# Optimization experiments

Hardware: AMD Instinct MI355X
Metric: run time of the kernel (lower is better)

## Reference

```python
import jax, jax.numpy as jnp
import numpy as np
import math

EPS = 1e-11

def _gaussian_kernel3():
    # fixed 3x3 gaussian, mean=(3-1)/2=1, variance=0.5^2
    coords = jnp.arange(3, dtype=jnp.float32)
    xg = jnp.tile(coords[None, :], (3, 1))  # x_cord.repeat(3).view(3,3)
    yg = xg.T
    variance = 0.25
    g = (1.0 / (2.0 * math.pi * variance)) * jnp.exp(-((xg - 1.0) ** 2 + (yg - 1.0) ** 2) / (2.0 * variance))
    return g  # (3,3)

def setup_inputs() -> dict:
    key = jax.random.key(0)
    k1, k2 = jax.random.split(key)
    b, cin, h, w = 8, 512, 16, 16
    cout = 128
    x = jax.random.normal(k1, (b, cin, h, w), dtype=jnp.float32)
    w_conv = jax.random.normal(k2, (cout, cin), dtype=jnp.float32) * (1.0 / np.sqrt(cin))
    return {"x": x, "w_conv": w_conv}

def reference(x, w_conv):
    # 1x1 conv (no bias) + relu
    y = jnp.einsum('bihw,oi->bohw', x, w_conv)
    y = jax.nn.relu(y)
    # depthwise 3x3 gaussian blur, VALID padding (matches nn.Conv2d default padding=0)
    c = w_conv.shape[0]
    gk = _gaussian_kernel3()
    dw = jnp.tile(gk[None, None], (c, 1, 1, 1))  # (C,1,3,3)
    y = jax.lax.conv_general_dilated(
        y, dw, window_strides=(1, 1), padding='VALID',
        dimension_numbers=('NCHW', 'OIHW', 'NCHW'), feature_group_count=c)
    b, c, h, w = y.shape
    hw = h * w
    xf = y.reshape(b, c, hw)
    # shifted copies: xs[b, ch, i, p] = xf[b, ch, (p - i) mod hw]
    p = jnp.arange(hw)
    idx = (p[None, :] - p[:, None]) % hw  # (hw_i, hw_p)
    xs = xf[:, :, idx]  # [b, c, hw, hw]
    # responses[b, ch1, ch2, p] = sum_i xf[b,ch1,i] * xf[b,ch2,(p-i)%hw]
    R = jnp.einsum('bai,bcip->bacp', xf, xs)  # [b, c, c, hw]
    # faithful torch reshape: [b, c, c*hw] -> view(b, hw, c*c), max over dim 1
    resp = R.reshape(b, hw, c * c)
    c_ij = jnp.sqrt(jnp.max(resp, axis=1))  # [b, c*c]
    norm = jnp.sum(c_ij ** 2, axis=1, keepdims=True) + EPS
    return c_ij / norm
```

## Files before the change

### kernel.cpp

```cpp
#include <hip/hip_runtime.h>
#include <hip/hip_bf16.h>

typedef __bf16 bf16x8 __attribute__((ext_vector_type(8)));
typedef float floatx4 __attribute__((ext_vector_type(4)));
typedef unsigned short u16;
typedef unsigned int u32;

#define HW 196
#define NB 8
#define NC 128
#define CL 480
#define WROW 12544

#define OFF_XFRSW 0
#define OFF_XFE   458752
#define OFF_W     8323072
#define OFF_SUMS  21168128
#define OFF_YPART 21168160

__global__ __launch_bounds__(512) void k_conv(const float* __restrict__ x,
                                              const float* __restrict__ wc,
                                              float* __restrict__ Ypart) {
  const int b  = blockIdx.x;
  const int og = blockIdx.y;
  const int ks = blockIdx.z;
  const int t  = threadIdx.x;
  const int pix  = t & 255;
  const int half = t >> 8;

  const float* xb = x + ((size_t)(b * 512 + ks * 64 + half * 32)) * 256 + pix;
  const float* wp = wc + (og * 16) * 512 + ks * 64 + half * 32;

  float acc[16];
#pragma unroll
  for (int r = 0; r < 16; ++r) acc[r] = 0.f;
#pragma unroll 8
  for (int i = 0; i < 32; ++i) {
    float xv = xb[(size_t)i * 256];
#pragma unroll
    for (int r = 0; r < 16; ++r) acc[r] = fmaf(xv, wp[r * 512 + i], acc[r]);
  }

  __shared__ float red[16][512];
#pragma unroll
  for (int r = 0; r < 16; ++r) red[r][t] = acc[r];
  __syncthreads();

  if (t < 256) {
    float* yo = Ypart + (((size_t)(b * 8 + og) * 8 + ks) * 16) * 256 + t;
#pragma unroll
    for (int r = 0; r < 16; ++r)
      yo[r * 256] = red[r][t] + red[r][t + 256];
  }
}

__global__ __launch_bounds__(256) void k_reduce(const float* __restrict__ Ypart,
                                                uint4* __restrict__ xfr_sw,
                                                u16* __restrict__ xfe) {
  const int b  = blockIdx.x;
  const int rg = blockIdx.y;
  const int t  = threadIdx.x;

  __shared__ float ybuf[4][256];
  __shared__ u16 ydup[4][592];

#pragma unroll
  for (int oo = 0; oo < 4; ++oo) {
    const int o  = rg * 4 + oo;
    const int og = o >> 4, r = o & 15;
    const float* yp = Ypart + (((size_t)(b * 8 + og) * 8) * 16 + r) * 256 + t;
    float s = 0.f;
#pragma unroll
    for (int ks = 0; ks < 8; ++ks) s += yp[(size_t)ks * 16 * 256];
    ybuf[oo][t] = fmaxf(s, 0.f);
  }
  __syncthreads();

  const float GC = 0.63661977236758138f;
  const float GE = GC * 0.13533528323661270f;
  const float GD = GC * 0.018315638888734179f;

  if (t < HW) {
    const int h = t / 14, w2 = t - h * 14;
#pragma unroll
    for (int oo = 0; oo < 4; ++oo) {
      const float* yb = &ybuf[oo][h * 16 + w2];
      float v = GD * (yb[0] + yb[2] + yb[32] + yb[34])
              + GE * (yb[1] + yb[16] + yb[18] + yb[33])
              + GC * yb[17];
      union { __hip_bfloat16 h2; u16 u; } cv; cv.h2 = __float2bfloat16(v);
      ydup[oo][t] = cv.u; ydup[oo][t + 196] = cv.u; ydup[oo][t + 392] = cv.u;
    }
  }
  __syncthreads();

  if (t < 112) {
    const int oo = t / 28;
    const int g  = t - oo * 28;
    const int kb = g >> 2, quad = g & 3;
    const int c  = rg * 4 + oo;
    const int at = c >> 4, m = c & 15;
    union { u16 u[8]; uint4 v; } pk;
#pragma unroll
    for (int j = 0; j < 8; ++j) {
      const int k = g * 8 + j;
      pk.u[j] = (k < HW) ? ydup[oo][HW - k] : (u16)0;
    }
    xfr_sw[b * 3584 + ((kb * 8 + at) * 4 + quad) * 16 + m] = pk.v;
  }

  uint4* xfe4 = (uint4*)xfe;
  for (int idx = t; idx < 4 * 8 * 60; idx += 256) {
    const int oo = idx / 480;
    const int rem = idx - oo * 480;
    const int S = rem / 60;
    const int g = rem - S * 60;
    const int c = rg * 4 + oo;
    union { u16 u[8]; uint4 v; } pk;
#pragma unroll
    for (int j = 0; j < 8; ++j) pk.u[j] = ydup[oo][g * 8 + j + S];
    xfe4[((size_t)(b * NC + c) * 8 + S) * 60 + g] = pk.v;
  }
}

__global__ __launch_bounds__(256, 2) void k_cooc(const uint4* __restrict__ xfr_sw,
                                                 const u16* __restrict__ xfe,
                                                 u32* __restrict__ W) {
  const int b     = blockIdx.x;
  const int cpair = blockIdx.y;
  const int t     = threadIdx.x;

  __shared__ __align__(16) uint4 Abuf[3584];
  __shared__ __align__(16) u16 Obuf[32 * 200];

  {
    const uint4* src = xfr_sw + b * 3584;
    for (int j = t; j < 3584; j += 256) Abuf[j] = src[j];
  }
  __syncthreads();

  const int lane = t & 63;
  const int wv   = t >> 6;
  const int n    = lane & 15;
  const int quad = lane >> 4;
  const u16* xbase = xfe + ((size_t)(b * NC) * 8) * CL + (n & 8) + quad * 8
                   + (size_t)(n & 7) * CL;

  for (int c2 = 0; c2 < 2; ++c2) {
    const int c = cpair * 2 + c2;
    const u16* xc = xbase + (size_t)c * (8 * CL);

    floatx4 acc[8][4];
#pragma unroll
    for (int at = 0; at < 8; ++at)
#pragma unroll
      for (int j = 0; j < 4; ++j) acc[at][j] = (floatx4){0.f, 0.f, 0.f, 0.f};

    for (int kb = 0; kb < 7; ++kb) {
      bf16x8 af[8];
#pragma unroll
      for (int at = 0; at < 8; ++at)
        af[at] = *((const bf16x8*)&Abuf[(kb * 8 + at) * 64 + lane]);

#define DO_PT(JC)                                                                \
      {                                                                          \
        const int p0 = (wv + 4 * (JC)) * 16;                                     \
        const bf16x8 bv = *((const bf16x8*)&xc[p0 + kb * 32]);                   \
        _Pragma("unroll")                                                        \
        for (int at = 0; at < 8; ++at)                                           \
          acc[at][JC] = __builtin_amdgcn_mfma_f32_16x16x32_bf16(af[at], bv,      \
                                                                acc[at][JC], 0, 0, 0); \
      }
      DO_PT(0)
      DO_PT(1)
      DO_PT(2)
      if (wv == 0) { DO_PT(3) }
#undef DO_PT
    }

#define EPI(JC)                                                                  \
    {                                                                            \
      const int p = (wv + 4 * (JC)) * 16 + n;                                    \
      if (p < HW) {                                                              \
        _Pragma("unroll")                                                        \
        for (int a0t = 0; a0t < 2; ++a0t) {                                      \
          _Pragma("unroll")                                                      \
          for (int rr = 0; rr < 4; ++rr) {                                       \
            float v = fmaxf(fmaxf(acc[a0t][JC][rr], acc[a0t + 2][JC][rr]),       \
                            fmaxf(acc[a0t + 4][JC][rr], acc[a0t + 6][JC][rr]));  \
            const int a1 = a0t * 16 + quad * 4 + rr;                             \
            union { __hip_bfloat16 h; u16 u; } cv;                               \
            cv.h = __float2bfloat16(v);                                          \
            Obuf[a1 * 200 + p] = cv.u;                                           \
          }                                                                      \
        }                                                                        \
      }                                                                          \
    }
    EPI(0)
    EPI(1)
    EPI(2)
    if (wv == 0) { EPI(3) }
#undef EPI
    __syncthreads();

    {
      const u32* O32 = (const u32*)Obuf;
      u32* Wb = W + ((size_t)b * 32) * WROW + c * 98;
      for (int j = t; j < 32 * 98; j += 256) {
        const int row = (int)(((unsigned)j * 10700u) >> 20);
        const int col = j - row * 98;
        Wb[row * WROW + col] = O32[row * 100 + col];
      }
    }
    __syncthreads();
  }
}

__global__ __launch_bounds__(256) void k_max(const u32* __restrict__ W,
                                             float* __restrict__ out,
                                             float* __restrict__ sums) {
  const int gid = blockIdx.x * 256 + threadIdx.x;
  const int b  = gid >> 13;
  const int r0 = (gid & 8191) << 1;
  const u32* Wb = W + (size_t)b * 32 * WROW;

  float m0 = 0.f, m1 = 0.f;
#pragma unroll 4
  for (int a1 = 0; a1 < 32; ++a1) {
    const int s = (r0 - ((a1 * 8704) & 16383)) & 16383;
    const u32 v = Wb[a1 * WROW + (s >> 1)];
    m0 = fmaxf(m0, __uint_as_float((v & 0xffffu) << 16));
    m1 = fmaxf(m1, __uint_as_float(v & 0xffff0000u));
    if (s < 8704) {
      const u32 v2 = Wb[a1 * WROW + ((s + 16384) >> 1)];
      m0 = fmaxf(m0, __uint_as_float((v2 & 0xffffu) << 16));
      m1 = fmaxf(m1, __uint_as_float(v2 & 0xffff0000u));
    }
  }
  const int o = b * 16384 + r0;
  out[o]     = sqrtf(m0);
  out[o + 1] = sqrtf(m1);

  float s2 = m0 + m1;
#pragma unroll
  for (int off = 32; off > 0; off >>= 1) s2 += __shfl_down(s2, off, 64);
  __shared__ float part[4];
  if ((threadIdx.x & 63) == 0) part[threadIdx.x >> 6] = s2;
  __syncthreads();
  if (threadIdx.x == 0)
    atomicAdd(&sums[b], part[0] + part[1] + part[2] + part[3]);
}

__global__ __launch_bounds__(256) void k_norm(const float* __restrict__ sums,
                                              float* __restrict__ out) {
  const int gid = blockIdx.x * 256 + threadIdx.x;
  const int b = gid >> 14;
  out[gid] = out[gid] / (sums[b] + 1e-11f);
}

extern "C" void kernel_launch(void* const* d_in, const int* in_sizes, int n_in,
                              void* d_out, int out_size, void* d_ws, size_t ws_size,
                              hipStream_t stream) {
  const float* x  = (const float*)d_in[0];
  const float* wc = (const float*)d_in[1];

  char* ws = (char*)d_ws;
  uint4* xfr_sw = (uint4*)(ws + OFF_XFRSW);
  u16*   xfe    = (u16*)(ws + OFF_XFE);
  u32*   W      = (u32*)(ws + OFF_W);
  float* sums   = (float*)(ws + OFF_SUMS);
  float* Ypart  = (float*)(ws + OFF_YPART);

  hipMemsetAsync(sums, 0, NB * sizeof(float), stream);
  k_conv<<<dim3(NB, 8, 8), 512, 0, stream>>>(x, wc, Ypart);
  k_reduce<<<dim3(NB, 32), 256, 0, stream>>>(Ypart, xfr_sw, xfe);
  k_cooc<<<dim3(NB, 64), 256, 0, stream>>>(xfr_sw, xfe, W);
  k_max<<<256, 256, 0, stream>>>(W, (float*)d_out, sums);
  k_norm<<<(NB * 16384) / 256, 256, 0, stream>>>(sums, (float*)d_out);
}
```

Before: 126.3 us.

## Replace fp32 split-K 1x1 conv with bf16 MFMA conv and fused relu

Adds a cast kernel that converts x into a pixel-major bf16 layout and w_conv into bf16. The 1x1 conv then runs on MFMA 16x16x32 bf16 instructions, with relu applied in the epilogue, and writes Y directly. This removes the split-K partial buffer and the reduction pass that the blur kernel used to do. The cost is an extra kernel launch, bf16 rounding of the conv inputs, and a conv grid of only 32 blocks, which leaves much of the GPU idle.

```diff
diff --git a/kernel.cpp b/kernel.cpp
--- a/kernel.cpp
+++ b/kernel.cpp
@@ -16,47 +16,85 @@
 #define OFF_XFE   458752
 #define OFF_W     8323072
 #define OFF_SUMS  21168128
-#define OFF_YPART 21168160
-
-__global__ __launch_bounds__(512) void k_conv(const float* __restrict__ x,
+#define OFF_Y     21168160
+#define OFF_XBT   22216736
+#define OFF_WB    24313888
+
+__global__ __launch_bounds__(256) void k_cast(const float* __restrict__ x,
                                               const float* __restrict__ wc,
-                                              float* __restrict__ Ypart) {
+                                              u16* __restrict__ xbT,
+                                              u16* __restrict__ wb) {
+  const int bid = blockIdx.x;
+  const int t   = threadIdx.x;
+  if (bid < 512) {
+    const int gid = bid * 256 + t;
+    const int pix = gid & 255;
+    const int kc  = (gid >> 8) & 63;
+    const int b   = gid >> 14;
+    union { u16 u[8]; uint4 v; } pk;
+#pragma unroll
+    for (int j = 0; j < 8; ++j) {
+      union { __hip_bfloat16 h; u16 u; } cv;
+      cv.h = __float2bfloat16(x[((size_t)(b * 512 + kc * 8 + j)) * 256 + pix]);
+      pk.u[j] = cv.u;
+    }
+    ((uint4*)xbT)[(size_t)(b * 256 + pix) * 64 + kc] = pk.v;
+  } else {
+    const int wid = (bid - 512) * 256 + t;
+    const float4* wf4 = (const float4*)wc;
+    const float4 f0 = wf4[wid * 2], f1 = wf4[wid * 2 + 1];
+    union { u16 u[8]; uint4 v; } pk;
+    union { __hip_bfloat16 h; u16 u; } cv;
+    cv.h = __float2bfloat16(f0.x); pk.u[0] = cv.u;
+    cv.h = __float2bfloat16(f0.y); pk.u[1] = cv.u;
+    cv.h = __float2bfloat16(f0.z); pk.u[2] = cv.u;
+    cv.h = __float2bfloat16(f0.w); pk.u[3] = cv.u;
+    cv.h = __float2bfloat16(f1.x); pk.u[4] = cv.u;
+    cv.h = __float2bfloat16(f1.y); pk.u[5] = cv.u;
+    cv.h = __float2bfloat16(f1.z); pk.u[6] = cv.u;
+    cv.h = __float2bfloat16(f1.w); pk.u[7] = cv.u;
+    ((uint4*)wb)[wid] = pk.v;
+  }
+}
+
+__global__ __launch_bounds__(256) void k_conv(const u16* __restrict__ xbT,
+                                              const u16* __restrict__ wb,
+                                              float* __restrict__ Y) {
   const int b  = blockIdx.x;
-  const int og = blockIdx.y;
-  const int ks = blockIdx.z;
+  const int pg = blockIdx.y;
   const int t  = threadIdx.x;
-  const int pix  = t & 255;
-  const int half = t >> 8;
-
-  const float* xb = x + ((size_t)(b * 512 + ks * 64 + half * 32)) * 256 + pix;
-  const float* wp = wc + (og * 16) * 512 + ks * 64 + half * 32;
-
-  float acc[16];
-#pragma unroll
-  for (int r = 0; r < 16; ++r) acc[r] = 0.f;
-#pragma unroll 8
-  for (int i = 0; i < 32; ++i) {
-    float xv = xb[(size_t)i * 256];
-#pragma unroll
-    for (int r = 0; r < 16; ++r) acc[r] = fmaf(xv, wp[r * 512 + i], acc[r]);
-  }
-
-  __shared__ float red[16][512];
-#pragma unroll
-  for (int r = 0; r < 16; ++r) red[r][t] = acc[r];
-  __syncthreads();
-
-  if (t < 256) {
-    float* yo = Ypart + (((size_t)(b * 8 + og) * 8 + ks) * 16) * 256 + t;
-#pragma unroll
-    for (int r = 0; r < 16; ++r)
-      yo[r * 256] = red[r][t] + red[r][t + 256];
-  }
-}
-
-__global__ __launch_bounds__(256) void k_reduce(const float* __restrict__ Ypart,
-                                                uint4* __restrict__ xfr_sw,
-                                                u16* __restrict__ xfe) {
+  const int lane = t & 63, wv = t >> 6;
+  const int n = lane & 15, quad = lane >> 4;
+  const int pix0 = pg * 64 + wv * 16;
+
+  const u16* xrow = xbT + ((size_t)(b * 256) + pix0 + n) * 512 + quad * 8;
+  const u16* wrow = wb + (size_t)n * 512 + quad * 8;
+
+  floatx4 acc[8];
+#pragma unroll
+  for (int at = 0; at < 8; ++at) acc[at] = (floatx4){0.f, 0.f, 0.f, 0.f};
+
+#pragma unroll 4
+  for (int kb = 0; kb < 16; ++kb) {
+    const bf16x8 bv = *(const bf16x8*)(xrow + kb * 32);
+#pragma unroll
+    for (int at = 0; at < 8; ++at) {
+      const bf16x8 av = *(const bf16x8*)(wrow + (size_t)(at * 16) * 512 + kb * 32);
+      acc[at] = __builtin_amdgcn_mfma_f32_16x16x32_bf16(av, bv, acc[at], 0, 0, 0);
+    }
+  }
+
+  float* Yb = Y + ((size_t)b * 128) * 256 + pix0 + n;
+#pragma unroll
+  for (int at = 0; at < 8; ++at)
+#pragma unroll
+    for (int rr = 0; rr < 4; ++rr)
+      Yb[(at * 16 + quad * 4 + rr) * 256] = fmaxf(acc[at][rr], 0.f);
+}
+
+__global__ __launch_bounds__(256) void k_blur(const float* __restrict__ Y,
+                                              uint4* __restrict__ xfr_sw,
+                                              u16* __restrict__ xfe) {
   const int b  = blockIdx.x;
   const int rg = blockIdx.y;
   const int t  = threadIdx.x;
@@ -65,15 +103,8 @@
   __shared__ u16 ydup[4][592];
 
 #pragma unroll
-  for (int oo = 0; oo < 4; ++oo) {
-    const int o  = rg * 4 + oo;
-    const int og = o >> 4, r = o & 15;
-    const float* yp = Ypart + (((size_t)(b * 8 + og) * 8) * 16 + r) * 256 + t;
-    float s = 0.f;
-#pragma unroll
-    for (int ks = 0; ks < 8; ++ks) s += yp[(size_t)ks * 16 * 256];
-    ybuf[oo][t] = fmaxf(s, 0.f);
-  }
+  for (int oo = 0; oo < 4; ++oo)
+    ybuf[oo][t] = Y[((size_t)(b * 128) + rg * 4 + oo) * 256 + t];
   __syncthreads();
 
   const float GC = 0.63661977236758138f;
@@ -269,11 +300,14 @@
   u16*   xfe    = (u16*)(ws + OFF_XFE);
   u32*   W      = (u32*)(ws + OFF_W);
   float* sums   = (float*)(ws + OFF_SUMS);
-  float* Ypart  = (float*)(ws + OFF_YPART);
+  float* Y      = (float*)(ws + OFF_Y);
+  u16*   xbT    = (u16*)(ws + OFF_XBT);
+  u16*   wb     = (u16*)(ws + OFF_WB);
 
   hipMemsetAsync(sums, 0, NB * sizeof(float), stream);
-  k_conv<<<dim3(NB, 8, 8), 512, 0, stream>>>(x, wc, Ypart);
-  k_reduce<<<dim3(NB, 32), 256, 0, stream>>>(Ypart, xfr_sw, xfe);
+  k_cast<<<544, 256, 0, stream>>>(x, wc, xbT, wb);
+  k_conv<<<dim3(NB, 4), 256, 0, stream>>>(xbT, wb, Y);
+  k_blur<<<dim3(NB, 32), 256, 0, stream>>>(Y, xfr_sw, xfe);
   k_cooc<<<dim3(NB, 64), 256, 0, stream>>>(xfr_sw, xfe, W);
   k_max<<<256, 256, 0, stream>>>(W, (float*)d_out, sums);
   k_norm<<<(NB * 16384) / 256, 256, 0, stream>>>(sums, (float*)d_out);
```

Measured after the change: 139.4 us. 1.1x slower.
